# Performance work log

Hardware: AMD Instinct MI355X
Metric: run time of the kernel (lower is better)

Reference implementation:

```python
import jax, jax.numpy as jnp
import numpy as np

Q_DIM = 1024
K_DIM = 768
N_HEADS = 16
HEAD_DIM = Q_DIM // N_HEADS
SCALE = HEAD_DIM ** -0.5


def setup_inputs() -> dict:
    key = jax.random.key(0)
    ks = jax.random.split(key, 11)
    B, N, M = 8, 1024, 1024
    s_q = 1.0 / np.sqrt(Q_DIM)
    s_k = 1.0 / np.sqrt(K_DIM)
    return {
        "query": jax.random.normal(ks[0], (B, N, Q_DIM), jnp.float32),
        "key": jax.random.normal(ks[1], (B, M, K_DIM), jnp.float32),
        "value": jax.random.normal(ks[2], (B, M, K_DIM), jnp.float32),
        # nn.Linear weights stored torch-style as [out, in]
        "w_q": jax.random.uniform(ks[3], (Q_DIM, Q_DIM), jnp.float32, -s_q, s_q),
        "b_q": jax.random.uniform(ks[4], (Q_DIM,), jnp.float32, -s_q, s_q),
        "w_k": jax.random.uniform(ks[5], (Q_DIM, K_DIM), jnp.float32, -s_k, s_k),
        "b_k": jax.random.uniform(ks[6], (Q_DIM,), jnp.float32, -s_k, s_k),
        "w_v": jax.random.uniform(ks[7], (Q_DIM, K_DIM), jnp.float32, -s_k, s_k),
        "b_v": jax.random.uniform(ks[8], (Q_DIM,), jnp.float32, -s_k, s_k),
        "w_o": jax.random.uniform(ks[9], (Q_DIM, Q_DIM), jnp.float32, -s_q, s_q),
        "b_o": jax.random.uniform(ks[10], (Q_DIM,), jnp.float32, -s_q, s_q),
    }


def reference(query, key, value, w_q, b_q, w_k, b_k, w_v, b_v, w_o, b_o):
    B, N, _ = query.shape
    M = key.shape[1]
    # projections (Linear: x @ W.T + b), split into heads -> [B, H, S, D]
    q = (query @ w_q.T + b_q).reshape(B, N, N_HEADS, HEAD_DIM).transpose(0, 2, 1, 3)
    k = (key @ w_k.T + b_k).reshape(B, M, N_HEADS, HEAD_DIM).transpose(0, 2, 1, 3)
    v = (value @ w_v.T + b_v).reshape(B, M, N_HEADS, HEAD_DIM).transpose(0, 2, 1, 3)
    # scaled dot-product attention, full [B, H, N, M] scores (matches original)
    scores = jnp.einsum("bhnd,bhmd->bhnm", q, k) * SCALE
    attn = jax.nn.softmax(scores, axis=-1)  # dropout is identity in eval mode
    out = jnp.einsum("bhnm,bhmd->bhnd", attn, v)
    out = out.transpose(0, 2, 1, 3).reshape(B, N, Q_DIM)
    out = out @ w_o.T + b_o
    return out, attn.mean(axis=1)
```

## Files before the change

### kernel.cpp

```cpp
#include <hip/hip_runtime.h>
#include <hip/hip_cooperative_groups.h>

namespace cg = cooperative_groups;


typedef float f32x4 __attribute__((ext_vector_type(4)));
typedef short bf16x8 __attribute__((ext_vector_type(8)));
typedef unsigned u32x2 __attribute__((ext_vector_type(2)));

#define QSCALE 0.18033688011112042f
#define PF 4

__device__ __forceinline__ short f2bf(float x) {
    union { float f; unsigned int u; } v;
    v.f = x;
    unsigned int r = v.u + 0x7FFFu + ((v.u >> 16) & 1u);
    return (short)(r >> 16);
}

__device__ __forceinline__ unsigned cvt_pk(float lo, float hi) {
    unsigned r;
    asm("v_cvt_pk_bf16_f32 %0, %1, %2" : "=v"(r) : "v"(lo), "v"(hi));
    return r;
}
__device__ __forceinline__ bf16x8 cvt8(float4 a0, float4 a1) {
    union { unsigned u[4]; bf16x8 v; } r;
    r.u[0] = cvt_pk(a0.x, a0.y);
    r.u[1] = cvt_pk(a0.z, a0.w);
    r.u[2] = cvt_pk(a1.x, a1.y);
    r.u[3] = cvt_pk(a1.z, a1.w);
    return r.v;
}

__device__ __forceinline__ f32x4 mfma_bf16(bf16x8 a, bf16x8 b, f32x4 c) {
    return __builtin_amdgcn_mfma_f32_16x16x32_bf16(a, b, c, 0, 0, 0);
}

__global__ __launch_bounds__(256) void wconv_kernel(
    const float* __restrict__ wq, const float* __restrict__ wk,
    const float* __restrict__ wv, const float* __restrict__ wo,
    short* __restrict__ wqb, short* __restrict__ wkb,
    short* __restrict__ wvb, short* __restrict__ wof)
{
    const int z = blockIdx.y;
    const int t = blockIdx.x * 256 + threadIdx.x;
    if (z == 0) {
        const float* p = wq + (size_t)t * 8;
        *(bf16x8*)(wqb + (size_t)t * 8) =
            cvt8(*(const float4*)p, *(const float4*)(p + 4));
    } else if (z == 3) {
        const int col = t >> 7, k8 = t & 127;
        const float* p = wo + (size_t)col * 1024 + k8 * 8;
        *(bf16x8*)(wof + ((col >> 4) * 16384 + k8 * 128 + (col & 15) * 8)) =
            cvt8(*(const float4*)p, *(const float4*)(p + 4));
    } else {
        if (t < 98304) {
            const float* src = (z == 1) ? wk : wv;
            short* dst = (z == 1) ? wkb : wvb;
            const float* p = src + (size_t)t * 8;
            *(bf16x8*)(dst + (size_t)t * 8) =
                cvt8(*(const float4*)p, *(const float4*)(p + 4));
        }
    }
}

template <int MODE>
__device__ __forceinline__ void proj_body(
    const float* __restrict__ Ain, const short* __restrict__ Wb,
    const float* __restrict__ bias, short* __restrict__ outb,
    short* sh)
{
    constexpr int KDIM = (MODE == 1 || MODE == 2) ? 768 : 1024;
    constexpr int NT = KDIM / 64;
    short* Alds = sh;
    short* Wlds = sh + 8192;

    const int tid  = threadIdx.x;
    const int lane = tid & 63;
    const int g = lane >> 4, c = lane & 15;
    const int wid = tid >> 6;
    const int wm = wid >> 1, wn = wid & 1;
    const int bn = blockIdx.y & 7;
    const int bm = blockIdx.x * 8 + (blockIdx.y >> 3);

    const int srow = tid >> 3;
    const int scol = (tid & 7) * 8;

    const float* Abase = Ain + (size_t)(bm * 128 + srow) * KDIM + scol;
    const short* Wbase = Wb + (size_t)(bn * 128 + srow) * KDIM + scol;

    f32x4 acc[4][4] = {};
    float4 Apre[2][2];
    bf16x8 Wpre[2];

    #pragma unroll
    for (int p = 0; p < 2; ++p) {
        const float* ap = Abase + (size_t)(p * 32) * KDIM;
        Apre[p][0] = *(const float4*)ap;
        Apre[p][1] = *(const float4*)(ap + 4);
        Wpre[p] = *(const bf16x8*)(Wbase + (size_t)(p * 32) * KDIM);
    }

    for (int kt = 0; kt < NT; ++kt) {
        const int k0 = kt * 64;
        __syncthreads();
        #pragma unroll
        for (int p = 0; p < 2; ++p) {
            const int r = p * 32 + srow;
            const int byt = (r * 128 + scol * 2) ^ ((r & 7) << 4);
            *(bf16x8*)((char*)Alds + byt) = cvt8(Apre[p][0], Apre[p][1]);
            *(bf16x8*)((char*)Wlds + byt) = Wpre[p];
        }
        if (kt + 1 < NT) {
            const int k0n = k0 + 64;
            #pragma unroll
            for (int p = 0; p < 2; ++p) {
                const float* ap = Abase + (size_t)(p * 32) * KDIM + k0n;
                Apre[p][0] = *(const float4*)ap;
                Apre[p][1] = *(const float4*)(ap + 4);
                Wpre[p] = *(const bf16x8*)(Wbase + (size_t)(p * 32) * KDIM + k0n);
            }
        }
        #pragma unroll
        for (int p = 2; p < 4; ++p) {
            const int r = p * 32 + srow;
            const float* ap = Abase + (size_t)(p * 32) * KDIM + k0;
            bf16x8 av = cvt8(*(const float4*)ap, *(const float4*)(ap + 4));
            bf16x8 wv8 = *(const bf16x8*)(Wbase + (size_t)(p * 32) * KDIM + k0);
            const int byt = (r * 128 + scol * 2) ^ ((r & 7) << 4);
            *(bf16x8*)((char*)Alds + byt) = av;
            *(bf16x8*)((char*)Wlds + byt) = wv8;
        }
        __syncthreads();
        #pragma unroll
        for (int kc = 0; kc < 2; ++kc) {
            bf16x8 af[4], bfr[4];
            #pragma unroll
            for (int t = 0; t < 4; ++t) {
                const int ra = wm * 64 + t * 16 + c;
                af[t]  = *(const bf16x8*)((const char*)Alds +
                          ((ra * 128 + (kc * 32 + g * 8) * 2) ^ ((ra & 7) << 4)));
                const int rb = wn * 64 + t * 16 + c;
                bfr[t] = *(const bf16x8*)((const char*)Wlds +
                          ((rb * 128 + (kc * 32 + g * 8) * 2) ^ ((rb & 7) << 4)));
            }
            #pragma unroll
            for (int i = 0; i < 4; ++i)
                #pragma unroll
                for (int j = 0; j < 4; ++j)
                    acc[i][j] = mfma_bf16(af[i], bfr[j], acc[i][j]);
        }
    }

    __syncthreads();
    #pragma unroll
    for (int j = 0; j < 4; ++j) {
        const int d = j * 16 + c;
        const float bv = bias[bn * 128 + wn * 64 + d];
        #pragma unroll
        for (int i = 0; i < 4; ++i) {
            #pragma unroll
            for (int r = 0; r < 4; ++r) {
                const int s = wm * 64 + i * 16 + g * 4 + r;
                float v = acc[i][j][r] + bv;
                if constexpr (MODE == 0) v *= QSCALE;
                int off;
                if constexpr (MODE == 0)
                    off = (s >> 4) * 1024 + (d >> 5) * 512 +
                          ((d >> 3) & 3) * 128 + (s & 15) * 8 + (d & 7);
                else if constexpr (MODE == 1)
                    off = (s >> 4) * 1024 + (d >> 3) * 128 + (s & 15) * 8 + (d & 7);
                else
                    off = (s >> 5) * 2048 + (d >> 4) * 512 +
                          ((s >> 3) & 3) * 128 + (d & 15) * 8 + (s & 7);
                sh[wn * 8192 + off] = f2bf(v);
            }
        }
    }
    __syncthreads();
    const int bglob = bm >> 3, bml = bm & 7;
    #pragma unroll
    for (int hl = 0; hl < 2; ++hl) {
        short* dst = outb + (size_t)(bglob * 16 + bn * 2 + hl) * 65536 + bml * 8192;
        #pragma unroll
        for (int k = 0; k < 4; ++k) {
            const int e = (k * 256 + tid) * 8;
            *(bf16x8*)(dst + e) = *(const bf16x8*)(sh + hl * 8192 + e);
        }
    }
}

__global__ __launch_bounds__(256, 4) void prep_kernel(
    const float* __restrict__ query, const float* __restrict__ key,
    const float* __restrict__ value,
    const short* __restrict__ wqb, const float* __restrict__ bq,
    const short* __restrict__ wkb, const float* __restrict__ bk,
    const short* __restrict__ wvb, const float* __restrict__ bv,
    short* __restrict__ qf, short* __restrict__ kf, short* __restrict__ vf)
{
    __shared__ short sh[16384];
    const int z = blockIdx.z;
    if (z == 0)      proj_body<0>(query, wqb, bq, qf, sh);
    else if (z == 1) proj_body<1>(key,   wkb, bk, kf, sh);
    else             proj_body<2>(value, wvb, bv, vf, sh);
}

__global__ __launch_bounds__(512, 2) void attn_kernel(
    const short* Qf, const short* Kf, const short* Vf,
    const short* Wof, const float* bo, float* outp)
{
    __shared__ alignas(16) short Ohlds[32 * 1024];
    __shared__ alignas(16) short pbufs[8 * 32 * 40];
    __shared__ alignas(16) short oaslb[2][8][32][72];
    __shared__ alignas(16) float red[2][2][16][8];

    const int tid  = threadIdx.x;
    const int lane = tid & 63;
    const int w = tid >> 6;
    const int g = lane >> 4, c = lane & 15;
    const int b = blockIdx.x & 7, qt = blockIdx.x >> 3;

    f32x4 am[2][8] = {};

    bf16x8 qfr[2][2], kA[8];
    {
        const size_t hb0 = (size_t)(b * 16) * 65536;
        #pragma unroll
        for (int at = 0; at < 2; ++at)
            #pragma unroll
            for (int kc = 0; kc < 2; ++kc)
                qfr[at][kc] = *(const bf16x8*)(Qf + hb0 +
                    (size_t)((qt * 2 + at) * 1024 + kc * 512 + g * 128 + c * 8));
        #pragma unroll
        for (int mt = 0; mt < PF; ++mt)
            kA[mt] = *(const bf16x8*)(Kf + hb0 +
                (size_t)((w * 8 + mt) * 1024 + g * 128 + c * 8));
    }

    for (int h = 0; h < 16; ++h) {
        const int par = h & 1;
        const size_t hb = (size_t)(b * 16 + h) * 65536;

        bf16x8 kB[8];
        #pragma unroll
        for (int mt = PF; mt < 8; ++mt)
            kA[mt] = *(const bf16x8*)(Kf + hb +
                (size_t)((w * 8 + mt) * 1024 + g * 128 + c * 8));
        #pragma unroll
        for (int mt = 0; mt < 8; ++mt)
            kB[mt] = *(const bf16x8*)(Kf + hb +
                (size_t)((w * 8 + mt) * 1024 + (4 + g) * 128 + c * 8));

        f32x4 p[2][8] = {};
        #pragma unroll
        for (int mt = 0; mt < 8; ++mt) {
            p[0][mt] = mfma_bf16(qfr[0][0], kA[mt], p[0][mt]);
            p[1][mt] = mfma_bf16(qfr[1][0], kA[mt], p[1][mt]);
        }
        #pragma unroll
        for (int mt = 0; mt < 8; ++mt) {
            p[0][mt] = mfma_bf16(qfr[0][1], kB[mt], p[0][mt]);
            p[1][mt] = mfma_bf16(qfr[1][1], kB[mt], p[1][mt]);
        }

        f32x4 rs[2] = {};
        #pragma unroll
        for (int at = 0; at < 2; ++at)
            #pragma unroll
            for (int mt = 0; mt < 8; ++mt) {
                f32x4 v = p[at][mt];
                #pragma unroll
                for (int r = 0; r < 4; ++r)
                    v[r] = __builtin_amdgcn_exp2f(v[r]);
                p[at][mt] = v;
                rs[at] += v;
            }
        #pragma unroll
        for (int off = 1; off < 16; off <<= 1)
            #pragma unroll
            for (int at = 0; at < 2; ++at)
                #pragma unroll
                for (int r = 0; r < 4; ++r)
                    rs[at][r] += __shfl_xor(rs[at][r], off);
        if (c == 0) {
            #pragma unroll
            for (int at = 0; at < 2; ++at)
                #pragma unroll
                for (int r = 0; r < 4; ++r)
                    red[par][at][g * 4 + r][w] = rs[at][r];
        }

        short* pbs = pbufs + w * 1280;
        f32x4 oa[2][4] = {};
        #pragma unroll
        for (int ks = 0; ks < 4; ++ks) {
            bf16x8 vfr[4];
            #pragma unroll
            for (int dt = 0; dt < 4; ++dt)
                vfr[dt] = *(const bf16x8*)(Vf + hb +
                    (size_t)(((w * 4 + ks) * 4 + dt) * 512 + g * 128 + c * 8));
            #pragma unroll
            for (int at = 0; at < 2; ++at)
                #pragma unroll
                for (int m2 = 0; m2 < 2; ++m2)
                    #pragma unroll
                    for (int r = 0; r < 4; ++r)
                        pbs[(at * 16 + g * 4 + r) * 40 + m2 * 16 + c] =
                            f2bf(p[at][ks * 2 + m2][r]);
            asm volatile("s_waitcnt lgkmcnt(0)" ::: "memory");
            bf16x8 pa[2];
            #pragma unroll
            for (int at = 0; at < 2; ++at)
                pa[at] = *(const bf16x8*)&pbs[(at * 16 + c) * 40 + g * 8];
            #pragma unroll
            for (int dt = 0; dt < 4; ++dt) {
                oa[0][dt] = mfma_bf16(pa[0], vfr[dt], oa[0][dt]);
                oa[1][dt] = mfma_bf16(pa[1], vfr[dt], oa[1][dt]);
            }
        }
        #pragma unroll
        for (int at = 0; at < 2; ++at)
            #pragma unroll
            for (int dt = 0; dt < 4; ++dt)
                #pragma unroll
                for (int r = 0; r < 4; ++r)
                    oaslb[par][w][at * 16 + g * 4 + r][dt * 16 + c] =
                        f2bf(oa[at][dt][r]);

        if (h < 15) {
            const size_t hbN = hb + 65536;
            #pragma unroll
            for (int at = 0; at < 2; ++at)
                #pragma unroll
                for (int kc = 0; kc < 2; ++kc)
                    qfr[at][kc] = *(const bf16x8*)(Qf + hbN +
                        (size_t)((qt * 2 + at) * 1024 + kc * 512 + g * 128 + c * 8));
            #pragma unroll
            for (int mt = 0; mt < PF; ++mt)
                kA[mt] = *(const bf16x8*)(Kf + hbN +
                    (size_t)((w * 8 + mt) * 1024 + g * 128 + c * 8));
        }

        __syncthreads();

        #pragma unroll
        for (int at = 0; at < 2; ++at) {
            f32x4 rv;
            #pragma unroll
            for (int r = 0; r < 4; ++r) {
                f32x4 s0 = *(const f32x4*)&red[par][at][g * 4 + r][0];
                f32x4 s1 = *(const f32x4*)&red[par][at][g * 4 + r][4];
                f32x4 ss = s0 + s1;
                rv[r] = 1.0f / (ss[0] + ss[1] + ss[2] + ss[3]);
            }
            #pragma unroll
            for (int mt = 0; mt < 8; ++mt)
                am[at][mt] += p[at][mt] * rv;
        }

        {
            const int zn = tid >> 4, zd = (tid & 15) * 4;
            const int zh = zn >> 4, zr = zn & 15;
            f32x4 s0 = *(const f32x4*)&red[par][zh][zr][0];
            f32x4 s1 = *(const f32x4*)&red[par][zh][zr][4];
            f32x4 ss = s0 + s1;
            const float inv = 1.0f / (ss[0] + ss[1] + ss[2] + ss[3]);
            f32x4 ov = {0.f, 0.f, 0.f, 0.f};
            #pragma unroll
            for (int i = 0; i < 8; ++i) {
                u32x2 uu = *(const u32x2*)&oaslb[par][i][zn][zd];
                union { unsigned u; float f; } e0, e1, e2, e3;
                e0.u = uu[0] << 16;  e1.u = uu[0] & 0xFFFF0000u;
                e2.u = uu[1] << 16;  e3.u = uu[1] & 0xFFFF0000u;
                ov[0] += e0.f; ov[1] += e1.f; ov[2] += e2.f; ov[3] += e3.f;
            }
            u32x2 pk;
            pk[0] = cvt_pk(ov[0] * inv, ov[1] * inv);
            pk[1] = cvt_pk(ov[2] * inv, ov[3] * inv);
            unsigned byt = (unsigned)(zn * 2048 + (h * 64 + zd) * 2);
            byt ^= (unsigned)((zn & 7) << 4);
            *(u32x2*)((char*)Ohlds + byt) = pk;
        }
    }

    __syncthreads();
    cg::this_grid().sync();

    float* aout = outp + 8388608 + (size_t)b * 1048576;
    #pragma unroll
    for (int at = 0; at < 2; ++at)
        #pragma unroll
        for (int mt = 0; mt < 8; ++mt)
            #pragma unroll
            for (int r = 0; r < 4; ++r) {
                const int n = qt * 32 + at * 16 + g * 4 + r;
                const int m = w * 128 + mt * 16 + c;
                aout[(size_t)n * 1024 + m] = am[at][mt][r] * 0.0625f;
            }

    f32x4 acc2[2][8] = {};
    for (int kt = 0; kt < 32; ++kt) {
        bf16x8 afr[2];
        #pragma unroll
        for (int at = 0; at < 2; ++at) {
            const int row = at * 16 + c;
            unsigned byt = (unsigned)(row * 2048 + (kt * 32 + g * 8) * 2);
            byt ^= (unsigned)((row & 7) << 4);
            afr[at] = *(const bf16x8*)((const char*)Ohlds + byt);
        }
        #pragma unroll
        for (int ct = 0; ct < 8; ++ct) {
            bf16x8 bfr = *(const bf16x8*)(Wof +
                ((w * 8 + ct) * 16384 + (kt * 4 + g) * 128 + c * 8));
            acc2[0][ct] = mfma_bf16(afr[0], bfr, acc2[0][ct]);
            acc2[1][ct] = mfma_bf16(afr[1], bfr, acc2[1][ct]);
        }
    }
    #pragma unroll
    for (int ct = 0; ct < 8; ++ct) {
        const int col = w * 128 + ct * 16 + c;
        const float bv = bo[col];
        #pragma unroll
        for (int at = 0; at < 2; ++at)
            #pragma unroll
            for (int r = 0; r < 4; ++r) {
                const int n = qt * 32 + at * 16 + g * 4 + r;
                outp[(size_t)(b * 1024 + n) * 1024 + col] = acc2[at][ct][r] + bv;
            }
    }
}

extern "C" void kernel_launch(void* const* d_in, const int* in_sizes, int n_in,
                              void* d_out, int out_size, void* d_ws, size_t ws_size,
                              hipStream_t stream)
{
    (void)in_sizes; (void)n_in; (void)out_size; (void)ws_size;
    const float* query = (const float*)d_in[0];
    const float* key   = (const float*)d_in[1];
    const float* value = (const float*)d_in[2];
    const float* w_q = (const float*)d_in[3];
    const float* b_q = (const float*)d_in[4];
    const float* w_k = (const float*)d_in[5];
    const float* b_k = (const float*)d_in[6];
    const float* w_v = (const float*)d_in[7];
    const float* b_v = (const float*)d_in[8];
    const float* w_o = (const float*)d_in[9];
    const float* b_o = (const float*)d_in[10];

    float* out = (float*)d_out;
    short* vf  = (short*)d_out;
    short* wqb = (short*)(out + 4194304);
    short* wkb = wqb + 1048576;
    short* wvb = wkb + 786432;
    short* qf  = (short*)(out + 8388608);
    short* kf  = qf + 8388608;
    short* wof = (short*)d_ws;

    wconv_kernel<<<dim3(512, 4), 256, 0, stream>>>(
        w_q, w_k, w_v, w_o, wqb, wkb, wvb, wof);

    prep_kernel<<<dim3(8, 64, 3), 256, 0, stream>>>(
        query, key, value, wqb, b_q, wkb, b_k, wvb, b_v, qf, kf, vf);

    void* args[] = { (void*)&qf, (void*)&kf, (void*)&vf,
                     (void*)&wof, (void*)&b_o, (void*)&out };
    hipLaunchCooperativeKernel(attn_kernel, dim3(256), dim3(512), args, 0u, stream);
}
```

Measured before the change: 241.3 us.

## Halve per-block query rows to launch 512 cooperative attention blocks

Templates the attention kernel on the number of 16-row query tiles per block (NAT) and launches 512 blocks of 16 rows with a 4-blocks-per-CU launch bound, falling back to the old 256-block, 32-row configuration if the cooperative launch fails. The aim is to fill more CUs (MI355X has 256) and raise occupancy, since 256 blocks left the GPU underpopulated. In exchange, K/V fragments and Wo reads are reused across half as many query rows, which roughly doubles their global/L2 traffic per output. Register pressure under the tighter launch bound also risks spills. The oaslb row padding is also changed from 72 to 68.

Result: slower. 406.1 us (+68.3%).

```diff
diff --git a/kernel.cpp b/kernel.cpp
--- a/kernel.cpp
+++ b/kernel.cpp
@@ -205,14 +205,15 @@
     else             proj_body<2>(value, wvb, bv, vf, sh);
 }
 
-__global__ __launch_bounds__(512, 2) void attn_kernel(
+template <int NAT>
+__global__ __launch_bounds__(512, (NAT == 1 ? 4 : 2)) void attn_kernel(
     const short* Qf, const short* Kf, const short* Vf,
     const short* Wof, const float* bo, float* outp)
 {
-    __shared__ alignas(16) short Ohlds[32 * 1024];
-    __shared__ alignas(16) short pbufs[8 * 32 * 40];
-    __shared__ alignas(16) short oaslb[2][8][32][72];
-    __shared__ alignas(16) float red[2][2][16][8];
+    __shared__ alignas(16) short Ohlds[NAT * 16 * 1024];
+    __shared__ alignas(16) short pbufs[8 * NAT * 16 * 40];
+    __shared__ alignas(16) short oaslb[2][8][NAT * 16][68];
+    __shared__ alignas(16) float red[2][NAT][16][8];
 
     const int tid  = threadIdx.x;
     const int lane = tid & 63;
@@ -220,17 +221,17 @@
     const int g = lane >> 4, c = lane & 15;
     const int b = blockIdx.x & 7, qt = blockIdx.x >> 3;
 
-    f32x4 am[2][8] = {};
-
-    bf16x8 qfr[2][2], kA[8];
+    f32x4 am[NAT][8] = {};
+
+    bf16x8 qfr[NAT][2], kA[8];
     {
         const size_t hb0 = (size_t)(b * 16) * 65536;
         #pragma unroll
-        for (int at = 0; at < 2; ++at)
+        for (int at = 0; at < NAT; ++at)
             #pragma unroll
             for (int kc = 0; kc < 2; ++kc)
                 qfr[at][kc] = *(const bf16x8*)(Qf + hb0 +
-                    (size_t)((qt * 2 + at) * 1024 + kc * 512 + g * 128 + c * 8));
+                    (size_t)((qt * NAT + at) * 1024 + kc * 512 + g * 128 + c * 8));
         #pragma unroll
         for (int mt = 0; mt < PF; ++mt)
             kA[mt] = *(const bf16x8*)(Kf + hb0 +
@@ -251,21 +252,21 @@
             kB[mt] = *(const bf16x8*)(Kf + hb +
                 (size_t)((w * 8 + mt) * 1024 + (4 + g) * 128 + c * 8));
 
-        f32x4 p[2][8] = {};
-        #pragma unroll
-        for (int mt = 0; mt < 8; ++mt) {
-            p[0][mt] = mfma_bf16(qfr[0][0], kA[mt], p[0][mt]);
-            p[1][mt] = mfma_bf16(qfr[1][0], kA[mt], p[1][mt]);
-        }
-        #pragma unroll
-        for (int mt = 0; mt < 8; ++mt) {
-            p[0][mt] = mfma_bf16(qfr[0][1], kB[mt], p[0][mt]);
-            p[1][mt] = mfma_bf16(qfr[1][1], kB[mt], p[1][mt]);
-        }
-
-        f32x4 rs[2] = {};
-        #pragma unroll
-        for (int at = 0; at < 2; ++at)
+        f32x4 p[NAT][8] = {};
+        #pragma unroll
+        for (int mt = 0; mt < 8; ++mt)
+            #pragma unroll
+            for (int at = 0; at < NAT; ++at)
+                p[at][mt] = mfma_bf16(qfr[at][0], kA[mt], p[at][mt]);
+        #pragma unroll
+        for (int mt = 0; mt < 8; ++mt)
+            #pragma unroll
+            for (int at = 0; at < NAT; ++at)
+                p[at][mt] = mfma_bf16(qfr[at][1], kB[mt], p[at][mt]);
+
+        f32x4 rs[NAT] = {};
+        #pragma unroll
+        for (int at = 0; at < NAT; ++at)
             #pragma unroll
             for (int mt = 0; mt < 8; ++mt) {
                 f32x4 v = p[at][mt];
@@ -278,20 +279,20 @@
         #pragma unroll
         for (int off = 1; off < 16; off <<= 1)
             #pragma unroll
-            for (int at = 0; at < 2; ++at)
+            for (int at = 0; at < NAT; ++at)
                 #pragma unroll
                 for (int r = 0; r < 4; ++r)
                     rs[at][r] += __shfl_xor(rs[at][r], off);
         if (c == 0) {
             #pragma unroll
-            for (int at = 0; at < 2; ++at)
+            for (int at = 0; at < NAT; ++at)
                 #pragma unroll
                 for (int r = 0; r < 4; ++r)
                     red[par][at][g * 4 + r][w] = rs[at][r];
         }
 
-        short* pbs = pbufs + w * 1280;
-        f32x4 oa[2][4] = {};
+        short* pbs = pbufs + w * (NAT * 16 * 40);
+        f32x4 oa[NAT][4] = {};
         #pragma unroll
         for (int ks = 0; ks < 4; ++ks) {
             bf16x8 vfr[4];
@@ -300,7 +301,7 @@
                 vfr[dt] = *(const bf16x8*)(Vf + hb +
                     (size_t)(((w * 4 + ks) * 4 + dt) * 512 + g * 128 + c * 8));
             #pragma unroll
-            for (int at = 0; at < 2; ++at)
+            for (int at = 0; at < NAT; ++at)
                 #pragma unroll
                 for (int m2 = 0; m2 < 2; ++m2)
                     #pragma unroll
@@ -308,18 +309,18 @@
                         pbs[(at * 16 + g * 4 + r) * 40 + m2 * 16 + c] =
                             f2bf(p[at][ks * 2 + m2][r]);
             asm volatile("s_waitcnt lgkmcnt(0)" ::: "memory");
-            bf16x8 pa[2];
-            #pragma unroll
-            for (int at = 0; at < 2; ++at)
+            bf16x8 pa[NAT];
+            #pragma unroll
+            for (int at = 0; at < NAT; ++at)
                 pa[at] = *(const bf16x8*)&pbs[(at * 16 + c) * 40 + g * 8];
             #pragma unroll
-            for (int dt = 0; dt < 4; ++dt) {
-                oa[0][dt] = mfma_bf16(pa[0], vfr[dt], oa[0][dt]);
-                oa[1][dt] = mfma_bf16(pa[1], vfr[dt], oa[1][dt]);
-            }
-        }
-        #pragma unroll
-        for (int at = 0; at < 2; ++at)
+            for (int dt = 0; dt < 4; ++dt)
+                #pragma unroll
+                for (int at = 0; at < NAT; ++at)
+                    oa[at][dt] = mfma_bf16(pa[at], vfr[dt], oa[at][dt]);
+        }
+        #pragma unroll
+        for (int at = 0; at < NAT; ++at)
             #pragma unroll
             for (int dt = 0; dt < 4; ++dt)
                 #pragma unroll
@@ -330,11 +331,11 @@
         if (h < 15) {
             const size_t hbN = hb + 65536;
             #pragma unroll
-            for (int at = 0; at < 2; ++at)
+            for (int at = 0; at < NAT; ++at)
                 #pragma unroll
                 for (int kc = 0; kc < 2; ++kc)
                     qfr[at][kc] = *(const bf16x8*)(Qf + hbN +
-                        (size_t)((qt * 2 + at) * 1024 + kc * 512 + g * 128 + c * 8));
+                        (size_t)((qt * NAT + at) * 1024 + kc * 512 + g * 128 + c * 8));
             #pragma unroll
             for (int mt = 0; mt < PF; ++mt)
                 kA[mt] = *(const bf16x8*)(Kf + hbN +
@@ -344,7 +345,7 @@
         __syncthreads();
 
         #pragma unroll
-        for (int at = 0; at < 2; ++at) {
+        for (int at = 0; at < NAT; ++at) {
             f32x4 rv;
             #pragma unroll
             for (int r = 0; r < 4; ++r) {
@@ -360,26 +361,28 @@
 
         {
             const int zn = tid >> 4, zd = (tid & 15) * 4;
-            const int zh = zn >> 4, zr = zn & 15;
-            f32x4 s0 = *(const f32x4*)&red[par][zh][zr][0];
-            f32x4 s1 = *(const f32x4*)&red[par][zh][zr][4];
-            f32x4 ss = s0 + s1;
-            const float inv = 1.0f / (ss[0] + ss[1] + ss[2] + ss[3]);
-            f32x4 ov = {0.f, 0.f, 0.f, 0.f};
-            #pragma unroll
-            for (int i = 0; i < 8; ++i) {
-                u32x2 uu = *(const u32x2*)&oaslb[par][i][zn][zd];
-                union { unsigned u; float f; } e0, e1, e2, e3;
-                e0.u = uu[0] << 16;  e1.u = uu[0] & 0xFFFF0000u;
-                e2.u = uu[1] << 16;  e3.u = uu[1] & 0xFFFF0000u;
-                ov[0] += e0.f; ov[1] += e1.f; ov[2] += e2.f; ov[3] += e3.f;
-            }
-            u32x2 pk;
-            pk[0] = cvt_pk(ov[0] * inv, ov[1] * inv);
-            pk[1] = cvt_pk(ov[2] * inv, ov[3] * inv);
-            unsigned byt = (unsigned)(zn * 2048 + (h * 64 + zd) * 2);
-            byt ^= (unsigned)((zn & 7) << 4);
-            *(u32x2*)((char*)Ohlds + byt) = pk;
+            if (zn < NAT * 16) {
+                const int zh = zn >> 4, zr = zn & 15;
+                f32x4 s0 = *(const f32x4*)&red[par][zh][zr][0];
+                f32x4 s1 = *(const f32x4*)&red[par][zh][zr][4];
+                f32x4 ss = s0 + s1;
+                const float inv = 1.0f / (ss[0] + ss[1] + ss[2] + ss[3]);
+                f32x4 ov = {0.f, 0.f, 0.f, 0.f};
+                #pragma unroll
+                for (int i = 0; i < 8; ++i) {
+                    u32x2 uu = *(const u32x2*)&oaslb[par][i][zn][zd];
+                    union { unsigned u; float f; } e0, e1, e2, e3;
+                    e0.u = uu[0] << 16;  e1.u = uu[0] & 0xFFFF0000u;
+                    e2.u = uu[1] << 16;  e3.u = uu[1] & 0xFFFF0000u;
+                    ov[0] += e0.f; ov[1] += e1.f; ov[2] += e2.f; ov[3] += e3.f;
+                }
+                u32x2 pk;
+                pk[0] = cvt_pk(ov[0] * inv, ov[1] * inv);
+                pk[1] = cvt_pk(ov[2] * inv, ov[3] * inv);
+                unsigned byt = (unsigned)(zn * 2048 + (h * 64 + zd) * 2);
+                byt ^= (unsigned)((zn & 7) << 4);
+                *(u32x2*)((char*)Ohlds + byt) = pk;
+            }
         }
     }
 
@@ -388,21 +391,21 @@
 
     float* aout = outp + 8388608 + (size_t)b * 1048576;
     #pragma unroll
-    for (int at = 0; at < 2; ++at)
+    for (int at = 0; at < NAT; ++at)
         #pragma unroll
         for (int mt = 0; mt < 8; ++mt)
             #pragma unroll
             for (int r = 0; r < 4; ++r) {
-                const int n = qt * 32 + at * 16 + g * 4 + r;
+                const int n = qt * NAT * 16 + at * 16 + g * 4 + r;
                 const int m = w * 128 + mt * 16 + c;
                 aout[(size_t)n * 1024 + m] = am[at][mt][r] * 0.0625f;
             }
 
-    f32x4 acc2[2][8] = {};
+    f32x4 acc2[NAT][8] = {};
     for (int kt = 0; kt < 32; ++kt) {
-        bf16x8 afr[2];
-        #pragma unroll
-        for (int at = 0; at < 2; ++at) {
+        bf16x8 afr[NAT];
+        #pragma unroll
+        for (int at = 0; at < NAT; ++at) {
             const int row = at * 16 + c;
             unsigned byt = (unsigned)(row * 2048 + (kt * 32 + g * 8) * 2);
             byt ^= (unsigned)((row & 7) << 4);
@@ -412,8 +415,9 @@
         for (int ct = 0; ct < 8; ++ct) {
             bf16x8 bfr = *(const bf16x8*)(Wof +
                 ((w * 8 + ct) * 16384 + (kt * 4 + g) * 128 + c * 8));
-            acc2[0][ct] = mfma_bf16(afr[0], bfr, acc2[0][ct]);
-            acc2[1][ct] = mfma_bf16(afr[1], bfr, acc2[1][ct]);
+            #pragma unroll
+            for (int at = 0; at < NAT; ++at)
+                acc2[at][ct] = mfma_bf16(afr[at], bfr, acc2[at][ct]);
         }
     }
     #pragma unroll
@@ -421,10 +425,10 @@
         const int col = w * 128 + ct * 16 + c;
         const float bv = bo[col];
         #pragma unroll
-        for (int at = 0; at < 2; ++at)
+        for (int at = 0; at < NAT; ++at)
             #pragma unroll
             for (int r = 0; r < 4; ++r) {
-                const int n = qt * 32 + at * 16 + g * 4 + r;
+                const int n = qt * NAT * 16 + at * 16 + g * 4 + r;
                 outp[(size_t)(b * 1024 + n) * 1024 + col] = acc2[at][ct][r] + bv;
             }
     }
@@ -464,5 +468,11 @@
 
     void* args[] = { (void*)&qf, (void*)&kf, (void*)&vf,
                      (void*)&wof, (void*)&b_o, (void*)&out };
-    hipLaunchCooperativeKernel(attn_kernel, dim3(256), dim3(512), args, 0u, stream);
-}
+    hipError_t e = hipLaunchCooperativeKernel(attn_kernel<1>, dim3(512),
+                                              dim3(512), args, 0u, stream);
+    if (e != hipSuccess) {
+        (void)hipGetLastError();
+        hipLaunchCooperativeKernel(attn_kernel<2>, dim3(256),
+                                   dim3(512), args, 0u, stream);
+    }
+}
```
